# Kernel tuning notes

Hardware: AMD Instinct MI355X
Metric: run time of the kernel (lower is better)

## Reference

```python
import jax, jax.numpy as jnp
import numpy as np
from jax import lax

B, T_IN, T_TASK = 1024, 512, 64
D_IN, D_TASK_FEAT, H, D_OUT = 9, 9, 100, 9


def setup_inputs() -> dict:
    key = jax.random.key(0)
    ks = jax.random.split(key, 8)
    s = 0.1
    return {
        "input": jax.random.normal(ks[0], (B, T_IN, D_IN), jnp.float32),
        "task": jax.random.normal(ks[1], (B, T_TASK, D_TASK_FEAT), jnp.float32),
        "W_in": jax.random.normal(ks[2], (D_IN, 9), jnp.float32) * s,
        "b_in": jnp.zeros((9,), jnp.float32),
        "W_task": jax.random.normal(ks[3], (D_TASK_FEAT, 9), jnp.float32) * s,
        "b_task": jnp.zeros((9,), jnp.float32),
        "W_x": jax.random.normal(ks[4], (9, 4 * H), jnp.float32) * s,
        "W_h": jax.random.normal(ks[5], (H, 4 * H), jnp.float32) * s,
        "b_lstm": jnp.zeros((4 * H,), jnp.float32),
        "W_out": jax.random.normal(ks[6], (H, D_OUT), jnp.float32) * s,
        "b_out": jnp.zeros((D_OUT,), jnp.float32),
    }


def reference(input, task, W_in, b_in, W_task, b_task, W_x, W_h, b_lstm, W_out, b_out):
    # Dense encoders with relu
    x = jax.nn.relu(jnp.einsum("btf,fd->btd", input, W_in) + b_in)      # [B,T1,9]
    t = jax.nn.relu(jnp.einsum("btf,fd->btd", task, W_task) + b_task)   # [B,T2,9]
    seq = jnp.concatenate([x, t], axis=1)                                # [B,T1+T2,9] (axis=1 = time)

    b = seq.shape[0]
    h0 = jnp.zeros((b, H), seq.dtype)
    c0 = jnp.zeros((b, H), seq.dtype)

    # Precompute input contributions for all timesteps (one big GEMM)
    zx = jnp.einsum("btf,fg->btg", seq, W_x) + b_lstm                    # [B,T,4H]

    def step(carry, zxt):
        h, c = carry
        z = zxt + h @ W_h                                                # [B,4H]
        i, f, g, o = jnp.split(z, 4, axis=-1)                            # Keras gate order i,f,c,o
        i = jax.nn.sigmoid(i)
        f = jax.nn.sigmoid(f)
        g = jnp.tanh(g)
        o = jax.nn.sigmoid(o)
        c = f * c + i * g
        h = o * jnp.tanh(c)
        return (h, c), h

    _, hs = lax.scan(step, (h0, c0), zx.transpose(1, 0, 2))              # hs: [T,B,H]
    hs = hs.transpose(1, 0, 2)                                           # [B,T,H]

    logits = jnp.einsum("bth,hd->btd", hs, W_out) + b_out
    return jax.nn.softmax(logits, axis=-1)
```

## Files before the change

### kernel.cpp

```cpp
#include <hip/hip_runtime.h>


#define NTHR 512

typedef _Float16 half8 __attribute__((ext_vector_type(8)));
typedef float    f32x4 __attribute__((ext_vector_type(4)));

struct __align__(16) SM {
  _Float16 Y[2][4][144];
};

__device__ __forceinline__ float fast_sigmoid(float x) {
  return __builtin_amdgcn_rcpf(1.f + __expf(-x));
}
__device__ __forceinline__ float fast_tanh(float x) {
  return fmaf(2.f, __builtin_amdgcn_rcpf(1.f + __expf(-2.f * x)), -1.f);
}

__device__ __forceinline__ float wld(int k, int n,
                                     const float* __restrict__ Wh,
                                     const float* __restrict__ Wx,
                                     const float* __restrict__ bl) {
  if (k < 100)  return Wh[k * 400 + n];
  if (k < 109)  return Wx[(k - 100) * 400 + n];
  if (k == 109) return bl[n];
  return 0.f;
}

__device__ __forceinline__ float wproj(int k, int m,
                                       const float* __restrict__ Wo,
                                       const float* __restrict__ bo) {
  if (m >= 9)   return 0.f;
  if (k < 100)  return Wo[k * 9 + m];
  if (k == 109) return bo[m];
  return 0.f;
}

__device__ __forceinline__ void sync_lds() {
  asm volatile("s_waitcnt lgkmcnt(0)" ::: "memory");
  __builtin_amdgcn_s_barrier();
  asm volatile("" ::: "memory");
}

__device__ __forceinline__ float swz_xor16(float v) {
  return __uint_as_float(__builtin_amdgcn_ds_swizzle(__float_as_uint(v), 0x401F));
}

__global__ __launch_bounds__(NTHR, 1)
void lstm_fused(const float* __restrict__ g_input,
                const float* __restrict__ g_task,
                const float* __restrict__ g_Win,
                const float* __restrict__ g_bin,
                const float* __restrict__ g_Wtask,
                const float* __restrict__ g_btask,
                const float* __restrict__ g_Wx,
                const float* __restrict__ g_Wh,
                const float* __restrict__ g_bl,
                const float* __restrict__ g_Wout,
                const float* __restrict__ g_bout,
                float* __restrict__ g_out)
{
  __shared__ SM L;
  const int tid  = threadIdx.x;
  const int bg0  = blockIdx.x * 4;
  const int wv   = tid >> 6;
  const int lane = tid & 63;
  const int q    = lane >> 4;
  const int nl   = lane & 15;
  const int hi   = lane >> 4;
  const int xr_  = nl >> 2;
  const int ab   = nl & 3;

  for (int i = tid; i < 2 * 4 * 144; i += NTHR)
    ((_Float16*)L.Y)[i] = ((i % 144) == 109) ? (_Float16)1.f : (_Float16)0.f;

  const int NT    = (wv < 2) ? 4 : 3;
  const int tbase = (wv < 2) ? wv * 4 : 8 + 3 * (wv - 2);
  const int NTact = (wv == 7) ? 2 : NT;

  half8 Af[4][4];
  {
    const int gate = ab;
    const int Uin  = xr_;
#pragma unroll
    for (int ti = 0; ti < 4; ++ti) {
      if (ti < NT) {
        const bool proj = (wv == 7 && ti == 2);
        const int n = gate * 100 + (tbase + ti) * 4 + Uin;
#pragma unroll
        for (int kc = 0; kc < 4; ++kc) {
#pragma unroll
          for (int j = 0; j < 8; ++j) {
            const int k = kc * 32 + q * 8 + j;
            Af[ti][kc][j] = (_Float16)(proj ? wproj(k, nl, g_Wout, g_bout)
                                            : wld(k, n, g_Wh, g_Wx, g_bl));
          }
        }
      }
    }
  }

  const int aU = (tbase + ((xr_ < NT) ? xr_ : NT - 1)) * 4 + hi;
  float c_state = 0.f;

  const int sl  = lane - 28;
  const int stb = (sl >= 0) ? sl / 9 : 0;
  const int stf = (sl >= 0) ? sl % 9 : 0;
  float we_in[9], we_task[9], be_in = 0.f, be_task = 0.f;
  if (wv == 6) {
#pragma unroll
    for (int ff = 0; ff < 9; ++ff) {
      we_in[ff]   = g_Win[ff * 9 + stf];
      we_task[ff] = g_Wtask[ff * 9 + stf];
    }
    be_in = g_bin[stf]; be_task = g_btask[stf];
  }
  float xrA[9], xrB[9];

  auto LOADX = [&](float* xr, int tt) {
    const float* src = (tt < 512)
      ? g_input + ((long)(bg0 + stb) * 512 + tt) * 9
      : g_task  + ((long)(bg0 + stb) * 64 + (tt - 512)) * 9;
#pragma unroll
    for (int ff = 0; ff < 9; ++ff) xr[ff] = src[ff];
  };
  auto ENC9 = [&](const float* xr, const float (&w)[9], float b) -> float {
    float a0 = b, a1 = 0.f, a2 = 0.f;
    a0 = fmaf(xr[0], w[0], a0); a1 = fmaf(xr[1], w[1], a1); a2 = fmaf(xr[2], w[2], a2);
    a0 = fmaf(xr[3], w[3], a0); a1 = fmaf(xr[4], w[4], a1); a2 = fmaf(xr[5], w[5], a2);
    a0 = fmaf(xr[6], w[6], a0); a1 = fmaf(xr[7], w[7], a1); a2 = fmaf(xr[8], w[8], a2);
    return (a0 + a1) + a2;
  };
  auto ENCSTEP = [&](const float* xr, int tt) {
    float a;
    if (tt < 512) a = ENC9(xr, we_in, be_in);
    else          a = ENC9(xr, we_task, be_task);
    L.Y[tt & 1][stb][100 + stf] = (_Float16)fmaxf(a, 0.f);
  };
  auto SMAX = [&](f32x4 v, int tout) {
    float e0 = __expf(v[0]), e1 = __expf(v[1]), e2 = __expf(v[2]), e3 = __expf(v[3]);
    if (hi == 2) { e1 = 0.f; e2 = 0.f; e3 = 0.f; }
    if (hi == 3) { e0 = 0.f; e1 = 0.f; e2 = 0.f; e3 = 0.f; }
    const float pl = (e0 + e1) + (e2 + e3);
    const float s1 = pl + swz_xor16(pl);
    const float ss = s1 + __shfl_xor(s1, 32, 64);
    const float rs = __builtin_amdgcn_rcpf(ss);
    if (hi < 3) {
      float* dst = g_out + ((long)(bg0 + ab) * 576 + tout) * 9 + 4 * hi;
      dst[0] = e0 * rs;
      if (hi < 2) { dst[1] = e1 * rs; dst[2] = e2 * rs; dst[3] = e3 * rs; }
    }
  };

  sync_lds();

  if (wv == 6 && sl >= 0) {
    float x0[9];
    LOADX(x0, 0);
    L.Y[0][stb][100 + stf] = (_Float16)fmaxf(ENC9(x0, we_in, be_in), 0.f);
    LOADX(xrB, 1);
    LOADX(xrA, 2);
  }
  sync_lds();

  for (int t = 0; t < 576; ++t) {
    const int p = t & 1;
    half8 Bv[4];
#pragma unroll
    for (int kc = 0; kc < 4; ++kc)
      Bv[kc] = *(const half8*)&L.Y[p][ab][kc * 32 + q * 8];
    f32x4 acc[4];
#pragma unroll
    for (int ti = 0; ti < 4; ++ti) {
      if (ti < NT) {
        acc[ti] = (f32x4)0.f;
#pragma unroll
        for (int kc = 0; kc < 4; ++kc)
          acc[ti] = __builtin_amdgcn_mfma_f32_16x16x32_f16(Af[ti][kc], Bv[kc], acc[ti], 0, 0, 0);
      }
    }
    if (NT == 3) acc[3] = acc[2];
    if (xr_ < NTact) {
      float zv[4];
#pragma unroll
      for (int g = 0; g < 4; ++g) {
        const float a01 = (xr_ == 0) ? acc[0][g] : acc[1][g];
        const float a23 = (xr_ == 2) ? acc[2][g] : acc[3][g];
        zv[g] = (xr_ < 2) ? a01 : a23;
      }
      const float gi = fast_sigmoid(zv[0]);
      const float gf = fast_sigmoid(zv[1]);
      const float gg = fast_tanh(zv[2]);
      const float go = fast_sigmoid(zv[3]);
      c_state = fmaf(gf, c_state, gi * gg);
      L.Y[p ^ 1][ab][aU] = (_Float16)(go * fast_tanh(c_state));
    } else if (wv == 7 && xr_ == 2) {
      if (t > 0) SMAX(acc[2], t - 1);
    }
    if (wv == 6 && sl >= 0 && t + 1 < 576) {
      if (t & 1) { ENCSTEP(xrA, t + 1); if (t + 3 < 576) LOADX(xrA, t + 3); }
      else       { ENCSTEP(xrB, t + 1); if (t + 3 < 576) LOADX(xrB, t + 3); }
    }
    sync_lds();
  }

  if (wv == 7) {
    half8 Bv[4];
#pragma unroll
    for (int kc = 0; kc < 4; ++kc)
      Bv[kc] = *(const half8*)&L.Y[0][ab][kc * 32 + q * 8];
    f32x4 a2 = (f32x4)0.f;
#pragma unroll
    for (int kc = 0; kc < 4; ++kc)
      a2 = __builtin_amdgcn_mfma_f32_16x16x32_f16(Af[2][kc], Bv[kc], a2, 0, 0, 0);
    if (xr_ == 2) SMAX(a2, 575);
  }
}

extern "C" void kernel_launch(void* const* d_in, const int* in_sizes, int n_in,
                              void* d_out, int out_size, void* d_ws, size_t ws_size,
                              hipStream_t stream) {
  const float* input  = (const float*)d_in[0];
  const float* task   = (const float*)d_in[1];
  const float* W_in   = (const float*)d_in[2];
  const float* b_in   = (const float*)d_in[3];
  const float* W_task = (const float*)d_in[4];
  const float* b_task = (const float*)d_in[5];
  const float* W_x    = (const float*)d_in[6];
  const float* W_h    = (const float*)d_in[7];
  const float* b_lstm = (const float*)d_in[8];
  const float* W_out  = (const float*)d_in[9];
  const float* b_out  = (const float*)d_in[10];
  float* out = (float*)d_out;

  lstm_fused<<<256, NTHR, 0, stream>>>(input, task, W_in, b_in, W_task, b_task,
                                       W_x, W_h, b_lstm, W_out, b_out, out);
}
```

Baseline: 471.8 us.

## Halve block to four waves with more tiles per wave and exp2-folded activations

Shrinks the block from eight waves to four. Each wave now owns six or seven MFMA tiles and updates two hidden units per lane, so the per-step barrier spans fewer waves. The weights are pre-scaled by -log2(e) (or -2·log2(e) for the cell gate), so gates use raw exp2 and shared reciprocals. This lowers transcendental and divide cost on the serial recurrence path. The trade-off is more serial MFMA and activation work per wave each step, and a small numerical change from the prescaling in fp16.

```diff
diff --git a/kernel.cpp b/kernel.cpp
--- a/kernel.cpp
+++ b/kernel.cpp
@@ -1,7 +1,8 @@
 #include <hip/hip_runtime.h>
 
 
-#define NTHR 512
+#define NTHR 256
+#define L2E 1.4426950408889634f
 
 typedef _Float16 half8 __attribute__((ext_vector_type(8)));
 typedef float    f32x4 __attribute__((ext_vector_type(4)));
@@ -10,11 +11,16 @@
   _Float16 Y[2][4][144];
 };
 
-__device__ __forceinline__ float fast_sigmoid(float x) {
-  return __builtin_amdgcn_rcpf(1.f + __expf(-x));
-}
-__device__ __forceinline__ float fast_tanh(float x) {
-  return fmaf(2.f, __builtin_amdgcn_rcpf(1.f + __expf(-2.f * x)), -1.f);
+__device__ __forceinline__ float fexp2(float x) {
+#if defined(__has_builtin)
+#if __has_builtin(__builtin_amdgcn_exp2f)
+  return __builtin_amdgcn_exp2f(x);
+#else
+  return __builtin_exp2f(x);
+#endif
+#else
+  return __builtin_exp2f(x);
+#endif
 }
 
 __device__ __forceinline__ float wld(int k, int n,
@@ -42,9 +48,8 @@
   asm volatile("" ::: "memory");
 }
 
-__device__ __forceinline__ float swz_xor16(float v) {
-  return __uint_as_float(__builtin_amdgcn_ds_swizzle(__float_as_uint(v), 0x401F));
-}
+#define SWZ_ADD(s, pat) \
+  (s) += __uint_as_float(__builtin_amdgcn_ds_swizzle(__float_as_uint(s), (pat)))
 
 __global__ __launch_bounds__(NTHR, 1)
 void lstm_fused(const float* __restrict__ g_input,
@@ -74,40 +79,41 @@
   for (int i = tid; i < 2 * 4 * 144; i += NTHR)
     ((_Float16*)L.Y)[i] = ((i % 144) == 109) ? (_Float16)1.f : (_Float16)0.f;
 
-  const int NT    = (wv < 2) ? 4 : 3;
-  const int tbase = (wv < 2) ? wv * 4 : 8 + 3 * (wv - 2);
-  const int NTact = (wv == 7) ? 2 : NT;
-
-  half8 Af[4][4];
+  const int NTF   = (wv == 0 || wv == 2) ? 7 : 6;
+  const int NR    = (wv == 3) ? 5 : NTF;
+  const int rem   = NR - 4;
+  const int tbase = (wv == 0) ? 0 : (wv == 1) ? 7 : (wv == 2) ? 13 : 20;
+
+  half8 Af[7][4];
   {
     const int gate = ab;
     const int Uin  = xr_;
-#pragma unroll
-    for (int ti = 0; ti < 4; ++ti) {
-      if (ti < NT) {
-        const bool proj = (wv == 7 && ti == 2);
+    const float scl = (gate == 2) ? (-2.f * L2E) : (-L2E);
+#pragma unroll
+    for (int ti = 0; ti < 7; ++ti) {
+      if (ti < NTF) {
+        const bool proj = (wv == 3 && ti == 5);
         const int n = gate * 100 + (tbase + ti) * 4 + Uin;
 #pragma unroll
         for (int kc = 0; kc < 4; ++kc) {
 #pragma unroll
           for (int j = 0; j < 8; ++j) {
             const int k = kc * 32 + q * 8 + j;
-            Af[ti][kc][j] = (_Float16)(proj ? wproj(k, nl, g_Wout, g_bout)
-                                            : wld(k, n, g_Wh, g_Wx, g_bl));
+            Af[ti][kc][j] = (_Float16)(proj ? wproj(k, nl, g_Wout, g_bout) * L2E
+                                            : wld(k, n, g_Wh, g_Wx, g_bl) * scl);
           }
         }
       }
     }
   }
 
-  const int aU = (tbase + ((xr_ < NT) ? xr_ : NT - 1)) * 4 + hi;
-  float c_state = 0.f;
+  float c0 = 0.f, c1 = 0.f;
 
   const int sl  = lane - 28;
   const int stb = (sl >= 0) ? sl / 9 : 0;
   const int stf = (sl >= 0) ? sl % 9 : 0;
   float we_in[9], we_task[9], be_in = 0.f, be_task = 0.f;
-  if (wv == 6) {
+  if (wv == 1) {
 #pragma unroll
     for (int ff = 0; ff < 9; ++ff) {
       we_in[ff]   = g_Win[ff * 9 + stf];
@@ -137,12 +143,24 @@
     else          a = ENC9(xr, we_task, be_task);
     L.Y[tt & 1][stb][100 + stf] = (_Float16)fmaxf(a, 0.f);
   };
+  auto ACT = [&](int p, const float* zv, int aUx, float& c) {
+    const float A = fexp2(zv[0]);
+    const float F = fexp2(zv[1]);
+    const float B = fexp2(zv[2]);
+    const float O = fexp2(zv[3]);
+    const float gf = __builtin_amdgcn_rcpf(1.f + F);
+    const float ig = (1.f - B) * __builtin_amdgcn_rcpf((1.f + A) * (1.f + B));
+    c = fmaf(gf, c, ig);
+    const float C = fexp2(fmaxf(c, -30.f) * (-2.f * L2E));
+    const float h = (1.f - C) * __builtin_amdgcn_rcpf((1.f + O) * (1.f + C));
+    L.Y[p ^ 1][ab][aUx] = (_Float16)h;
+  };
   auto SMAX = [&](f32x4 v, int tout) {
-    float e0 = __expf(v[0]), e1 = __expf(v[1]), e2 = __expf(v[2]), e3 = __expf(v[3]);
+    float e0 = fexp2(v[0]), e1 = fexp2(v[1]), e2 = fexp2(v[2]), e3 = fexp2(v[3]);
     if (hi == 2) { e1 = 0.f; e2 = 0.f; e3 = 0.f; }
     if (hi == 3) { e0 = 0.f; e1 = 0.f; e2 = 0.f; e3 = 0.f; }
     const float pl = (e0 + e1) + (e2 + e3);
-    const float s1 = pl + swz_xor16(pl);
+    const float s1 = pl + __uint_as_float(__builtin_amdgcn_ds_swizzle(__float_as_uint(pl), 0x401F));
     const float ss = s1 + __shfl_xor(s1, 32, 64);
     const float rs = __builtin_amdgcn_rcpf(ss);
     if (hi < 3) {
@@ -154,7 +172,7 @@
 
   sync_lds();
 
-  if (wv == 6 && sl >= 0) {
+  if (wv == 1 && sl >= 0) {
     float x0[9];
     LOADX(x0, 0);
     L.Y[0][stb][100 + stf] = (_Float16)fmaxf(ENC9(x0, we_in, be_in), 0.f);
@@ -169,18 +187,17 @@
 #pragma unroll
     for (int kc = 0; kc < 4; ++kc)
       Bv[kc] = *(const half8*)&L.Y[p][ab][kc * 32 + q * 8];
-    f32x4 acc[4];
-#pragma unroll
-    for (int ti = 0; ti < 4; ++ti) {
-      if (ti < NT) {
+    f32x4 acc[7];
+#pragma unroll
+    for (int ti = 0; ti < 7; ++ti) {
+      if (ti < NTF) {
         acc[ti] = (f32x4)0.f;
 #pragma unroll
         for (int kc = 0; kc < 4; ++kc)
           acc[ti] = __builtin_amdgcn_mfma_f32_16x16x32_f16(Af[ti][kc], Bv[kc], acc[ti], 0, 0, 0);
       }
     }
-    if (NT == 3) acc[3] = acc[2];
-    if (xr_ < NTact) {
+    {
       float zv[4];
 #pragma unroll
       for (int g = 0; g < 4; ++g) {
@@ -188,23 +205,27 @@
         const float a23 = (xr_ == 2) ? acc[2][g] : acc[3][g];
         zv[g] = (xr_ < 2) ? a01 : a23;
       }
-      const float gi = fast_sigmoid(zv[0]);
-      const float gf = fast_sigmoid(zv[1]);
-      const float gg = fast_tanh(zv[2]);
-      const float go = fast_sigmoid(zv[3]);
-      c_state = fmaf(gf, c_state, gi * gg);
-      L.Y[p ^ 1][ab][aU] = (_Float16)(go * fast_tanh(c_state));
-    } else if (wv == 7 && xr_ == 2) {
-      if (t > 0) SMAX(acc[2], t - 1);
-    }
-    if (wv == 6 && sl >= 0 && t + 1 < 576) {
+      ACT(p, zv, (tbase + xr_) * 4 + hi, c0);
+    }
+    if (xr_ < rem) {
+      float zv[4];
+#pragma unroll
+      for (int g = 0; g < 4; ++g) {
+        if (rem == 3)      zv[g] = (xr_ == 0) ? acc[4][g] : ((xr_ == 1) ? acc[5][g] : acc[6][g]);
+        else if (rem == 2) zv[g] = (xr_ == 0) ? acc[4][g] : acc[5][g];
+        else               zv[g] = acc[4][g];
+      }
+      ACT(p, zv, (tbase + 4 + xr_) * 4 + hi, c1);
+    }
+    if (wv == 3 && xr_ == 3 && t > 0) SMAX(acc[5], t - 1);
+    if (wv == 1 && sl >= 0 && t + 1 < 576) {
       if (t & 1) { ENCSTEP(xrA, t + 1); if (t + 3 < 576) LOADX(xrA, t + 3); }
       else       { ENCSTEP(xrB, t + 1); if (t + 3 < 576) LOADX(xrB, t + 3); }
     }
     sync_lds();
   }
 
-  if (wv == 7) {
+  if (wv == 3) {
     half8 Bv[4];
 #pragma unroll
     for (int kc = 0; kc < 4; ++kc)
@@ -212,8 +233,8 @@
     f32x4 a2 = (f32x4)0.f;
 #pragma unroll
     for (int kc = 0; kc < 4; ++kc)
-      a2 = __builtin_amdgcn_mfma_f32_16x16x32_f16(Af[2][kc], Bv[kc], a2, 0, 0, 0);
-    if (xr_ == 2) SMAX(a2, 575);
+      a2 = __builtin_amdgcn_mfma_f32_16x16x32_f16(Af[5][kc], Bv[kc], a2, 0, 0, 0);
+    if (xr_ == 3) SMAX(a2, 575);
   }
 }
 
```

Measured after the change: 916.7 us. +94.3%, slower.

## Split LSTM recurrence across sixteen waves with two tiles each

Applied to the files above, without the earlier changes.

Doubles the block to 1024 threads so each recurrent wave computes at most two 16-wide gate tiles instead of three or four. This halves the serial MFMA chain per timestep. The input encoder and the output projection/softmax each get their own dedicated wave (14 and 15). The cost is a barrier across twice as many waves every step. The launch-bounds hint now asks for four blocks per CU, which may tighten the register budget and cause spills.

```diff
diff --git a/kernel.cpp b/kernel.cpp
--- a/kernel.cpp
+++ b/kernel.cpp
@@ -1,7 +1,7 @@
 #include <hip/hip_runtime.h>
 
 
-#define NTHR 512
+#define NTHR 1024
 
 typedef _Float16 half8 __attribute__((ext_vector_type(8)));
 typedef float    f32x4 __attribute__((ext_vector_type(4)));
@@ -42,11 +42,7 @@
   asm volatile("" ::: "memory");
 }
 
-__device__ __forceinline__ float swz_xor16(float v) {
-  return __uint_as_float(__builtin_amdgcn_ds_swizzle(__float_as_uint(v), 0x401F));
-}
-
-__global__ __launch_bounds__(NTHR, 1)
+__global__ __launch_bounds__(NTHR, 4)
 void lstm_fused(const float* __restrict__ g_input,
                 const float* __restrict__ g_task,
                 const float* __restrict__ g_Win,
@@ -74,18 +70,18 @@
   for (int i = tid; i < 2 * 4 * 144; i += NTHR)
     ((_Float16*)L.Y)[i] = ((i % 144) == 109) ? (_Float16)1.f : (_Float16)0.f;
 
-  const int NT    = (wv < 2) ? 4 : 3;
-  const int tbase = (wv < 2) ? wv * 4 : 8 + 3 * (wv - 2);
-  const int NTact = (wv == 7) ? 2 : NT;
-
-  half8 Af[4][4];
+  const int NR    = (wv < 12) ? 2 : (wv == 12) ? 1 : 0;
+  const int NTF   = (wv == 15) ? 1 : NR;
+  const int tbase = (wv < 12) ? wv * 2 : 24;
+
+  half8 Af[2][4];
   {
     const int gate = ab;
     const int Uin  = xr_;
 #pragma unroll
-    for (int ti = 0; ti < 4; ++ti) {
-      if (ti < NT) {
-        const bool proj = (wv == 7 && ti == 2);
+    for (int ti = 0; ti < 2; ++ti) {
+      if (ti < NTF) {
+        const bool proj = (wv == 15);
         const int n = gate * 100 + (tbase + ti) * 4 + Uin;
 #pragma unroll
         for (int kc = 0; kc < 4; ++kc) {
@@ -100,14 +96,14 @@
     }
   }
 
-  const int aU = (tbase + ((xr_ < NT) ? xr_ : NT - 1)) * 4 + hi;
+  const int aU = (tbase + ((NR == 2) ? (xr_ & 1) : 0)) * 4 + hi;
   float c_state = 0.f;
 
   const int sl  = lane - 28;
   const int stb = (sl >= 0) ? sl / 9 : 0;
   const int stf = (sl >= 0) ? sl % 9 : 0;
   float we_in[9], we_task[9], be_in = 0.f, be_task = 0.f;
-  if (wv == 6) {
+  if (wv == 14) {
 #pragma unroll
     for (int ff = 0; ff < 9; ++ff) {
       we_in[ff]   = g_Win[ff * 9 + stf];
@@ -137,12 +133,20 @@
     else          a = ENC9(xr, we_task, be_task);
     L.Y[tt & 1][stb][100 + stf] = (_Float16)fmaxf(a, 0.f);
   };
+  auto ACT = [&](int p, const float* zv) {
+    const float gi = fast_sigmoid(zv[0]);
+    const float gf = fast_sigmoid(zv[1]);
+    const float gg = fast_tanh(zv[2]);
+    const float go = fast_sigmoid(zv[3]);
+    c_state = fmaf(gf, c_state, gi * gg);
+    L.Y[p ^ 1][ab][aU] = (_Float16)(go * fast_tanh(c_state));
+  };
   auto SMAX = [&](f32x4 v, int tout) {
     float e0 = __expf(v[0]), e1 = __expf(v[1]), e2 = __expf(v[2]), e3 = __expf(v[3]);
     if (hi == 2) { e1 = 0.f; e2 = 0.f; e3 = 0.f; }
     if (hi == 3) { e0 = 0.f; e1 = 0.f; e2 = 0.f; e3 = 0.f; }
     const float pl = (e0 + e1) + (e2 + e3);
-    const float s1 = pl + swz_xor16(pl);
+    const float s1 = pl + __uint_as_float(__builtin_amdgcn_ds_swizzle(__float_as_uint(pl), 0x401F));
     const float ss = s1 + __shfl_xor(s1, 32, 64);
     const float rs = __builtin_amdgcn_rcpf(ss);
     if (hi < 3) {
@@ -154,7 +158,7 @@
 
   sync_lds();
 
-  if (wv == 6 && sl >= 0) {
+  if (wv == 14 && sl >= 0) {
     float x0[9];
     LOADX(x0, 0);
     L.Y[0][stb][100 + stf] = (_Float16)fmaxf(ENC9(x0, we_in, be_in), 0.f);
@@ -166,54 +170,50 @@
   for (int t = 0; t < 576; ++t) {
     const int p = t & 1;
     half8 Bv[4];
-#pragma unroll
-    for (int kc = 0; kc < 4; ++kc)
-      Bv[kc] = *(const half8*)&L.Y[p][ab][kc * 32 + q * 8];
-    f32x4 acc[4];
-#pragma unroll
-    for (int ti = 0; ti < 4; ++ti) {
-      if (ti < NT) {
-        acc[ti] = (f32x4)0.f;
-#pragma unroll
-        for (int kc = 0; kc < 4; ++kc)
-          acc[ti] = __builtin_amdgcn_mfma_f32_16x16x32_f16(Af[ti][kc], Bv[kc], acc[ti], 0, 0, 0);
-      }
-    }
-    if (NT == 3) acc[3] = acc[2];
-    if (xr_ < NTact) {
-      float zv[4];
-#pragma unroll
-      for (int g = 0; g < 4; ++g) {
-        const float a01 = (xr_ == 0) ? acc[0][g] : acc[1][g];
-        const float a23 = (xr_ == 2) ? acc[2][g] : acc[3][g];
-        zv[g] = (xr_ < 2) ? a01 : a23;
-      }
-      const float gi = fast_sigmoid(zv[0]);
-      const float gf = fast_sigmoid(zv[1]);
-      const float gg = fast_tanh(zv[2]);
-      const float go = fast_sigmoid(zv[3]);
-      c_state = fmaf(gf, c_state, gi * gg);
-      L.Y[p ^ 1][ab][aU] = (_Float16)(go * fast_tanh(c_state));
-    } else if (wv == 7 && xr_ == 2) {
-      if (t > 0) SMAX(acc[2], t - 1);
-    }
-    if (wv == 6 && sl >= 0 && t + 1 < 576) {
-      if (t & 1) { ENCSTEP(xrA, t + 1); if (t + 3 < 576) LOADX(xrA, t + 3); }
-      else       { ENCSTEP(xrB, t + 1); if (t + 3 < 576) LOADX(xrB, t + 3); }
+    f32x4 acc[2];
+    if (NTF > 0) {
+#pragma unroll
+      for (int kc = 0; kc < 4; ++kc)
+        Bv[kc] = *(const half8*)&L.Y[p][ab][kc * 32 + q * 8];
+#pragma unroll
+      for (int ti = 0; ti < 2; ++ti) {
+        if (ti < NTF) {
+          acc[ti] = (f32x4)0.f;
+#pragma unroll
+          for (int kc = 0; kc < 4; ++kc)
+            acc[ti] = __builtin_amdgcn_mfma_f32_16x16x32_f16(Af[ti][kc], Bv[kc], acc[ti], 0, 0, 0);
+        }
+      }
+    }
+    if (NR > 0) {
+      if (xr_ < NR) {
+        float zv[4];
+#pragma unroll
+        for (int g = 0; g < 4; ++g)
+          zv[g] = (NR == 2 && (xr_ & 1)) ? acc[1][g] : acc[0][g];
+        ACT(p, zv);
+      }
+    } else if (wv == 15) {
+      if (xr_ == 0 && t > 0) SMAX(acc[0], t - 1);
+    } else if (wv == 14) {
+      if (sl >= 0 && t + 1 < 576) {
+        if (t & 1) { ENCSTEP(xrA, t + 1); if (t + 3 < 576) LOADX(xrA, t + 3); }
+        else       { ENCSTEP(xrB, t + 1); if (t + 3 < 576) LOADX(xrB, t + 3); }
+      }
     }
     sync_lds();
   }
 
-  if (wv == 7) {
+  if (wv == 15) {
     half8 Bv[4];
 #pragma unroll
     for (int kc = 0; kc < 4; ++kc)
       Bv[kc] = *(const half8*)&L.Y[0][ab][kc * 32 + q * 8];
-    f32x4 a2 = (f32x4)0.f;
+    f32x4 a0 = (f32x4)0.f;
 #pragma unroll
     for (int kc = 0; kc < 4; ++kc)
-      a2 = __builtin_amdgcn_mfma_f32_16x16x32_f16(Af[2][kc], Bv[kc], a2, 0, 0, 0);
-    if (xr_ == 2) SMAX(a2, 575);
+      a0 = __builtin_amdgcn_mfma_f32_16x16x32_f16(Af[0][kc], Bv[kc], a0, 0, 0, 0);
+    if (xr_ == 0) SMAX(a0, 575);
   }
 }
 
```

Result: faster. 437.3 us (-7.3%).
